# Kernel tuning notes

Hardware: AMD Instinct MI355X
Metric: run time of the kernel (lower is better)

Reference implementation:

```python
import jax, jax.numpy as jnp
import numpy as np

IN_DIM = 1024
OUT_DIM = 1024
NUM_EXPERTS = 8
TOP_K = 2
B = 8192


def setup_inputs() -> dict:
    key = jax.random.key(0)
    ks = jax.random.split(key, 8)
    s_in = 1.0 / np.sqrt(IN_DIM)
    s_out = 1.0 / np.sqrt(OUT_DIM)
    return {
        "x": jax.random.normal(ks[0], (B, IN_DIM), dtype=jnp.float32),
        # router Linear(in_dim, num_experts)
        "rw": jax.random.uniform(ks[1], (IN_DIM, NUM_EXPERTS), jnp.float32, -s_in, s_in),
        "rb": jax.random.uniform(ks[2], (NUM_EXPERTS,), jnp.float32, -s_in, s_in),
        # expert MLPs stacked along expert axis
        "w1": jax.random.uniform(ks[3], (NUM_EXPERTS, IN_DIM, OUT_DIM), jnp.float32, -s_in, s_in),
        "b1": jax.random.uniform(ks[4], (NUM_EXPERTS, OUT_DIM), jnp.float32, -s_in, s_in),
        "w2": jax.random.uniform(ks[5], (NUM_EXPERTS, OUT_DIM, OUT_DIM), jnp.float32, -s_out, s_out),
        "b2": jax.random.uniform(ks[6], (NUM_EXPERTS, OUT_DIM), jnp.float32, -s_out, s_out),
    }


def reference(x, rw, rb, w1, b1, w2, b2):
    # ---- TopkRouter ----
    logits = x @ rw + rb                                  # [B, E]
    topk_vals, topk_idx = jax.lax.top_k(logits, TOP_K)    # [B, K]
    neg_inf = jnp.full_like(logits, -jnp.inf)
    rows = jnp.arange(logits.shape[0])[:, None]
    sparse_logits = neg_inf.at[rows, topk_idx].set(topk_vals)
    gating = jax.nn.softmax(sparse_logits, axis=-1)       # zeros outside top-k

    # ---- experts: dense compute, gating weights are exactly 0 for
    # non-selected experts so the weighted combine matches the masked
    # dispatch of the original module. ----
    h = jax.nn.relu(jnp.einsum('bi,eio->beo', x, w1) + b1[None])   # [B, E, out]
    y = jnp.einsum('beh,eho->beo', h, w2) + b2[None]               # [B, E, out]
    fused = jnp.einsum('beo,be->bo', y, gating)                    # [B, out]
    return fused, gating
```

## Files before the change

### kernel.cpp

```cpp
#include <hip/hip_runtime.h>
#include <hip/hip_bf16.h>
#include <cstdint>
#include <cstddef>

#define IN_DIM 1024
#define OUT_DIM 1024
#define NE 8
#define NTOK 8192

typedef __bf16 bf16x8 __attribute__((ext_vector_type(8)));
typedef float f32x4 __attribute__((ext_vector_type(4)));

__device__ __forceinline__ unsigned short f2bf(float f) {
    unsigned u = __float_as_uint(f);
    unsigned r = 0x7fffu + ((u >> 16) & 1u);
    return (unsigned short)((u + r) >> 16);
}

__device__ __forceinline__ void bf2x(unsigned u, float& lo, float& hi) {
    lo = __uint_as_float(u << 16);
    hi = __uint_as_float(u & 0xffff0000u);
}

__device__ __forceinline__ void async16(void* lds, const void* g) {
    __builtin_amdgcn_global_load_lds(
        (const __attribute__((address_space(1))) unsigned int*)g,
        (__attribute__((address_space(3))) unsigned int*)lds,
        16, 0, 0);
}

__global__ __launch_bounds__(256) void convert_transpose_kernel(
    const float* __restrict__ w1, const float* __restrict__ w2,
    unsigned short* __restrict__ w1T, unsigned short* __restrict__ w2T) {
    __shared__ float tile[64][68];
    int z = blockIdx.z;
    const float* src = (z < 8) ? (w1 + (size_t)z * IN_DIM * OUT_DIM)
                               : (w2 + (size_t)(z - 8) * OUT_DIM * OUT_DIM);
    unsigned short* dst = (z < 8) ? (w1T + (size_t)z * IN_DIM * OUT_DIM)
                                  : (w2T + (size_t)(z - 8) * OUT_DIM * OUT_DIM);
    int kt = blockIdx.x * 64, nt = blockIdx.y * 64;
    int t = threadIdx.x;
    int r = t >> 2, cq = (t & 3) * 16;
#pragma unroll
    for (int q = 0; q < 4; ++q) {
        float4 v = *(const float4*)(src + (size_t)(kt + r) * 1024 + nt + cq + q * 4);
        tile[r][cq + q * 4 + 0] = v.x;
        tile[r][cq + q * 4 + 1] = v.y;
        tile[r][cq + q * 4 + 2] = v.z;
        tile[r][cq + q * 4 + 3] = v.w;
    }
    __syncthreads();
    int n = t >> 2, kq = (t & 3) * 16;
#pragma unroll
    for (int q = 0; q < 4; ++q) {
        ushort4 o;
        o.x = f2bf(tile[kq + q * 4 + 0][n]);
        o.y = f2bf(tile[kq + q * 4 + 1][n]);
        o.z = f2bf(tile[kq + q * 4 + 2][n]);
        o.w = f2bf(tile[kq + q * 4 + 3][n]);
        *(ushort4*)(dst + (size_t)(nt + n) * 1024 + kt + kq + q * 4) = o;
    }
}

__global__ __launch_bounds__(256) void router_kernel(
    const float* __restrict__ x, const float* __restrict__ rw,
    const float* __restrict__ rb,
    unsigned short* __restrict__ xb,
    float* __restrict__ gating, int* __restrict__ enc,
    float2* __restrict__ gw) {
    __shared__ float srw[NE * IN_DIM];
    int t = threadIdx.x;
#pragma unroll
    for (int i = 0; i < 4; ++i) {
        int k = t + i * 256;
        float4 a = *(const float4*)(rw + (size_t)k * NE);
        float4 b = *(const float4*)(rw + (size_t)k * NE + 4);
        srw[0 * IN_DIM + k] = a.x; srw[1 * IN_DIM + k] = a.y;
        srw[2 * IN_DIM + k] = a.z; srw[3 * IN_DIM + k] = a.w;
        srw[4 * IN_DIM + k] = b.x; srw[5 * IN_DIM + k] = b.y;
        srw[6 * IN_DIM + k] = b.z; srw[7 * IN_DIM + k] = b.w;
    }
    __syncthreads();
    int wave = t >> 6, lane = t & 63;
    int tok = blockIdx.x * 4 + wave;
    const float* xrow = x + (size_t)tok * IN_DIM;
    unsigned short* xbrow = xb + (size_t)tok * IN_DIM;
    float acc[NE] = {0, 0, 0, 0, 0, 0, 0, 0};
#pragma unroll
    for (int i = 0; i < 4; ++i) {
        int k = i * 256 + lane * 4;
        float4 xv = *(const float4*)(xrow + k);
        ushort4 o;
        o.x = f2bf(xv.x); o.y = f2bf(xv.y); o.z = f2bf(xv.z); o.w = f2bf(xv.w);
        *(ushort4*)(xbrow + k) = o;
#pragma unroll
        for (int e = 0; e < NE; ++e) {
            float4 wv = *(const float4*)(srw + e * IN_DIM + k);
            acc[e] = fmaf(xv.x, wv.x, fmaf(xv.y, wv.y, fmaf(xv.z, wv.z, fmaf(xv.w, wv.w, acc[e]))));
        }
    }
#pragma unroll
    for (int e = 0; e < NE; ++e) {
#pragma unroll
        for (int off = 32; off > 0; off >>= 1) acc[e] += __shfl_xor(acc[e], off);
        acc[e] += rb[e];
    }
    int e0 = 0; float v0 = acc[0];
#pragma unroll
    for (int e = 1; e < NE; ++e) if (acc[e] > v0) { v0 = acc[e]; e0 = e; }
    int e1 = -1; float v1 = -3.4e38f;
#pragma unroll
    for (int e = 0; e < NE; ++e) if (e != e0 && acc[e] > v1) { v1 = acc[e]; e1 = e; }
    float tg = __expf(v1 - v0);
    float inv = 1.0f / (1.0f + tg);
    float g0 = inv, g1 = tg * inv;
    if (lane < NE) gating[(size_t)tok * NE + lane] = (lane == e0) ? g0 : ((lane == e1) ? g1 : 0.0f);
    if (lane == 0) {
        enc[tok] = e0 | (e1 << 8);
        gw[tok] = make_float2(g0, g1);
    }
}

__global__ __launch_bounds__(1024) void bucket_kernel(
    const int* __restrict__ enc,
    int* __restrict__ bidx, int* __restrict__ slots, int* __restrict__ cnt) {
    int e = blockIdx.x;
    __shared__ int wsum[16];
    __shared__ int runbase;
    int t = threadIdx.x, wave = t >> 6, lane = t & 63;
    if (t == 0) runbase = 0;
    __syncthreads();
    for (int c0 = 0; c0 < NTOK; c0 += 1024) {
        int tok = c0 + t;
        int v = enc[tok];
        int e0 = v & 0xff, e1 = (v >> 8) & 0xff;
        bool sel = (e0 == e) || (e1 == e);
        unsigned long long m = __ballot(sel);
        int pos = __popcll(m & ((1ull << lane) - 1ull));
        if (lane == 0) wsum[wave] = __popcll(m);
        __syncthreads();
        int wb = runbase;
        for (int w = 0; w < wave; ++w) wb += wsum[w];
        if (sel) {
            int p = wb + pos;
            bidx[e * NTOK + p] = tok;
            int which = (e0 == e) ? 0 : 1;
            slots[2 * tok + which] = (e << 13) | p;
        }
        __syncthreads();
        if (t == 0) {
            int s = 0;
#pragma unroll
            for (int w = 0; w < 16; ++w) s += wsum[w];
            runbase += s;
        }
        __syncthreads();
    }
    if (t == 0) cnt[e] = runbase;
}

__device__ __forceinline__ int prefix_cnt(const int* __restrict__ cnt, int e) {
    int s = 0;
    for (int i = 0; i < NE; ++i) s += (i < e) ? cnt[i] : 0;
    return s;
}


__global__ __launch_bounds__(256) void gemm1_kernel(
    const unsigned short* __restrict__ xb, const unsigned short* __restrict__ w1T,
    const float* __restrict__ b1, const int* __restrict__ bidx,
    const int* __restrict__ cnt,
    unsigned short* __restrict__ H) {
    int b = blockIdx.x;
    int e = b & 7;
    int t2 = b >> 3;
    int nt = t2 & 7;
    int mt = t2 >> 3;
    int n_e = cnt[e];
    if (mt * 128 >= n_e) return;
    __shared__ __attribute__((aligned(16))) unsigned short As[2][64 * 64];
    __shared__ __attribute__((aligned(16))) unsigned short Bs[2][64 * 64];
    int t = threadIdx.x, wave = t >> 6, lane = t & 63;
    const int* be = bidx + e * NTOK;
    const unsigned short* agp[2]; const unsigned short* bgp[2];
    int ldsoff[2];
#pragma unroll
    for (int is = 0; is < 2; ++is) {
        int c = is * 256 + t;
        int line = c >> 3;
        int chunkg = (c & 7) ^ (line & 7);
        int growl = 2 * line + (chunkg >> 2);
        int gcol = (chunkg & 3) * 8;
        int gra = mt * 128 + growl;
        int grac = gra < n_e ? gra : n_e - 1;
        agp[is] = xb + (size_t)be[grac] * IN_DIM + gcol;
        bgp[is] = w1T + ((size_t)e * OUT_DIM + nt * 128 + growl) * IN_DIM + gcol;
        ldsoff[is] = (is * 256 + wave * 64) * 8;
    }
    int wm = wave & 1, wn = wave >> 1;
    int quad = lane >> 4, l15 = lane & 15;
    int lhalf = l15 >> 1;
    int slot = (((l15 & 1) * 4 + quad) ^ lhalf) * 8;
    f32x4 zero4 = {0.f, 0.f, 0.f, 0.f};
    f32x4 acc[4][4];
#pragma unroll
    for (int i = 0; i < 4; ++i)
#pragma unroll
        for (int j = 0; j < 4; ++j) acc[i][j] = zero4;

#pragma unroll
    for (int is = 0; is < 2; ++is) {
        async16(&As[0][ldsoff[is]], agp[is]);
        async16(&Bs[0][ldsoff[is]], bgp[is]);
    }
    for (int it = 0; it < 32; ++it) {
        __syncthreads();
        int buf = it & 1;
        if (it + 1 < 32) {
            int ktn = (it + 1) * 32;
#pragma unroll
            for (int is = 0; is < 2; ++is) {
                async16(&As[buf ^ 1][ldsoff[is]], agp[is] + ktn);
                async16(&Bs[buf ^ 1][ldsoff[is]], bgp[is] + ktn);
            }
        }
        const unsigned short* Ab = As[buf];
        const unsigned short* Bb = Bs[buf];
        bf16x8 av[4], bv[4];
#pragma unroll
        for (int i = 0; i < 4; ++i) {
            int lineA = wm * 32 + i * 8 + lhalf;
            av[i] = *(const bf16x8*)(Ab + lineA * 64 + slot);
        }
#pragma unroll
        for (int j = 0; j < 4; ++j) {
            int lineB = wn * 32 + j * 8 + lhalf;
            bv[j] = *(const bf16x8*)(Bb + lineB * 64 + slot);
        }
#pragma unroll
        for (int i = 0; i < 4; ++i)
#pragma unroll
            for (int j = 0; j < 4; ++j)
                acc[i][j] = __builtin_amdgcn_mfma_f32_16x16x32_bf16(av[i], bv[j], acc[i][j], 0, 0, 0);
    }
    int hbase = prefix_cnt(cnt, e);
    const float* b1e = b1 + (size_t)e * OUT_DIM;
    int n0 = nt * 128 + wn * 64 + l15;
#pragma unroll
    for (int j = 0; j < 4; ++j) {
        int n = n0 + j * 16;
        float bias = b1e[n];
#pragma unroll
        for (int i = 0; i < 4; ++i) {
            int m0 = mt * 128 + wm * 64 + i * 16 + quad * 4;
#pragma unroll
            for (int r = 0; r < 4; ++r) {
                int gm = m0 + r;
                if (gm < n_e) {
                    float h = acc[i][j][r] + bias;
                    h = h > 0.f ? h : 0.f;
                    H[(size_t)(hbase + gm) * OUT_DIM + n] = f2bf(h);
                }
            }
        }
    }
}

__global__ __launch_bounds__(256) void gemm2_kernel(
    const unsigned short* __restrict__ H, const unsigned short* __restrict__ w2T,
    const int* __restrict__ cnt,
    unsigned short* __restrict__ Y) {
    int b = blockIdx.x;
    int e = b & 7;
    int t2 = b >> 3;
    int nt = t2 & 7;
    int mt = t2 >> 3;
    int n_e = cnt[e];
    if (mt * 128 >= n_e) return;
    __shared__ __attribute__((aligned(16))) unsigned short As[2][64 * 64];
    __shared__ __attribute__((aligned(16))) unsigned short Bs[2][64 * 64];
    int t = threadIdx.x, wave = t >> 6, lane = t & 63;
    int hbase = prefix_cnt(cnt, e);
    const unsigned short* agp[2]; const unsigned short* bgp[2];
    int ldsoff[2];
#pragma unroll
    for (int is = 0; is < 2; ++is) {
        int c = is * 256 + t;
        int line = c >> 3;
        int chunkg = (c & 7) ^ (line & 7);
        int growl = 2 * line + (chunkg >> 2);
        int gcol = (chunkg & 3) * 8;
        int gra = mt * 128 + growl;
        int grac = gra < n_e ? gra : n_e - 1;
        agp[is] = H + (size_t)(hbase + grac) * OUT_DIM + gcol;
        bgp[is] = w2T + ((size_t)e * OUT_DIM + nt * 128 + growl) * OUT_DIM + gcol;
        ldsoff[is] = (is * 256 + wave * 64) * 8;
    }
    int wm = wave & 1, wn = wave >> 1;
    int quad = lane >> 4, l15 = lane & 15;
    int lhalf = l15 >> 1;
    int slot = (((l15 & 1) * 4 + quad) ^ lhalf) * 8;
    f32x4 zero4 = {0.f, 0.f, 0.f, 0.f};
    f32x4 acc[4][4];
#pragma unroll
    for (int i = 0; i < 4; ++i)
#pragma unroll
        for (int j = 0; j < 4; ++j) acc[i][j] = zero4;

#pragma unroll
    for (int is = 0; is < 2; ++is) {
        async16(&As[0][ldsoff[is]], agp[is]);
        async16(&Bs[0][ldsoff[is]], bgp[is]);
    }
    for (int it = 0; it < 32; ++it) {
        __syncthreads();
        int buf = it & 1;
        if (it + 1 < 32) {
            int ktn = (it + 1) * 32;
#pragma unroll
            for (int is = 0; is < 2; ++is) {
                async16(&As[buf ^ 1][ldsoff[is]], agp[is] + ktn);
                async16(&Bs[buf ^ 1][ldsoff[is]], bgp[is] + ktn);
            }
        }
        const unsigned short* Ab = As[buf];
        const unsigned short* Bb = Bs[buf];
        bf16x8 av[4], bv[4];
#pragma unroll
        for (int i = 0; i < 4; ++i) {
            int lineA = wm * 32 + i * 8 + lhalf;
            av[i] = *(const bf16x8*)(Ab + lineA * 64 + slot);
        }
#pragma unroll
        for (int j = 0; j < 4; ++j) {
            int lineB = wn * 32 + j * 8 + lhalf;
            bv[j] = *(const bf16x8*)(Bb + lineB * 64 + slot);
        }
#pragma unroll
        for (int i = 0; i < 4; ++i)
#pragma unroll
            for (int j = 0; j < 4; ++j)
                acc[i][j] = __builtin_amdgcn_mfma_f32_16x16x32_bf16(av[i], bv[j], acc[i][j], 0, 0, 0);
    }
    int n0 = nt * 128 + wn * 64 + l15;
#pragma unroll
    for (int i = 0; i < 4; ++i) {
        int m0 = mt * 128 + wm * 64 + i * 16 + quad * 4;
#pragma unroll
        for (int r = 0; r < 4; ++r) {
            int gm = m0 + r;
            if (gm < n_e) {
                unsigned short* yrow = Y + (size_t)(hbase + gm) * OUT_DIM;
#pragma unroll
                for (int j = 0; j < 4; ++j)
                    yrow[n0 + j * 16] = f2bf(acc[i][j][r]);
            }
        }
    }
}

__global__ __launch_bounds__(256) void combine_kernel(
    const unsigned short* __restrict__ Y, const float* __restrict__ b2,
    const float2* __restrict__ gw, const int* __restrict__ slots,
    const int* __restrict__ cnt, float* __restrict__ out) {
    int t = threadIdx.x, wave = t >> 6, lane = t & 63;
    int tok = blockIdx.x * 4 + wave;
    int pre[NE];
    {
        int s = 0;
#pragma unroll
        for (int i = 0; i < NE; ++i) { pre[i] = s; s += cnt[i]; }
    }
    int s0 = slots[2 * tok], s1 = slots[2 * tok + 1];
    int e0 = s0 >> 13, e1 = s1 >> 13;
    int r0 = pre[e0] + (s0 & 8191);
    int r1 = pre[e1] + (s1 & 8191);
    float2 g = gw[tok];
    const unsigned short* y0 = Y + (size_t)r0 * OUT_DIM;
    const unsigned short* y1 = Y + (size_t)r1 * OUT_DIM;
    const float* c0 = b2 + (size_t)e0 * OUT_DIM;
    const float* c1 = b2 + (size_t)e1 * OUT_DIM;
    float* orow = out + (size_t)tok * OUT_DIM;
#pragma unroll
    for (int i = 0; i < 2; ++i) {
        int c = i * 512 + lane * 8;
        uint4 ua = *(const uint4*)(y0 + c);
        uint4 ub = *(const uint4*)(y1 + c);
        float a[8], b[8];
        bf2x(ua.x, a[0], a[1]); bf2x(ua.y, a[2], a[3]);
        bf2x(ua.z, a[4], a[5]); bf2x(ua.w, a[6], a[7]);
        bf2x(ub.x, b[0], b[1]); bf2x(ub.y, b[2], b[3]);
        bf2x(ub.z, b[4], b[5]); bf2x(ub.w, b[6], b[7]);
        float4 p0 = *(const float4*)(c0 + c);
        float4 p1 = *(const float4*)(c0 + c + 4);
        float4 q0 = *(const float4*)(c1 + c);
        float4 q1 = *(const float4*)(c1 + c + 4);
        float o[8];
        o[0] = g.x * (a[0] + p0.x) + g.y * (b[0] + q0.x);
        o[1] = g.x * (a[1] + p0.y) + g.y * (b[1] + q0.y);
        o[2] = g.x * (a[2] + p0.z) + g.y * (b[2] + q0.z);
        o[3] = g.x * (a[3] + p0.w) + g.y * (b[3] + q0.w);
        o[4] = g.x * (a[4] + p1.x) + g.y * (b[4] + q1.x);
        o[5] = g.x * (a[5] + p1.y) + g.y * (b[5] + q1.y);
        o[6] = g.x * (a[6] + p1.z) + g.y * (b[6] + q1.z);
        o[7] = g.x * (a[7] + p1.w) + g.y * (b[7] + q1.w);
        *(float4*)(orow + c) = make_float4(o[0], o[1], o[2], o[3]);
        *(float4*)(orow + c + 4) = make_float4(o[4], o[5], o[6], o[7]);
    }
}

extern "C" void kernel_launch(void* const* d_in, const int* in_sizes, int n_in,
                              void* d_out, int out_size, void* d_ws, size_t ws_size,
                              hipStream_t stream) {
    const float* x  = (const float*)d_in[0];
    const float* rw = (const float*)d_in[1];
    const float* rb = (const float*)d_in[2];
    const float* w1 = (const float*)d_in[3];
    const float* b1 = (const float*)d_in[4];
    const float* w2 = (const float*)d_in[5];
    const float* b2 = (const float*)d_in[6];
    float* out = (float*)d_out;
    float* gating = out + (size_t)NTOK * OUT_DIM;

    char* ws = (char*)d_ws;
    unsigned short* xb  = (unsigned short*)(ws + 0);
    unsigned short* Y   = (unsigned short*)(ws + 0);
    unsigned short* w1T = (unsigned short*)(ws + 16777216);
    unsigned short* w2T = (unsigned short*)(ws + 33554432);
    unsigned short* H   = (unsigned short*)(ws + 50331648);
    int*   bidx  = (int*)(ws + 83886080);
    int*   slots = (int*)(ws + 84148224);
    int*   cnt   = (int*)(ws + 84213760);
    int*    enc  = (int*)(ws + 84213888);
    float2* gw   = (float2*)(ws + 84246656);

    convert_transpose_kernel<<<dim3(16, 16, 16), 256, 0, stream>>>(w1, w2, w1T, w2T);
    router_kernel<<<NTOK / 4, 256, 0, stream>>>(x, rw, rb, xb, gating, enc, gw);
    bucket_kernel<<<NE, 1024, 0, stream>>>(enc, bidx, slots, cnt);
    gemm1_kernel<<<8 * 8 * 64, 256, 0, stream>>>(xb, w1T, b1, bidx, cnt, H);
    gemm2_kernel<<<8 * 8 * 64, 256, 0, stream>>>(H, w2T, cnt, Y);
    combine_kernel<<<NTOK / 4, 256, 0, stream>>>(Y, b2, gw, slots, cnt, out);
    (void)in_sizes; (void)n_in; (void)out_size; (void)ws_size;
}
```

Before: 310.6 us.

## Parallelize expert bucketing with atomics and vectorize GEMM epilogue stores

The bucket kernel changes from one block per expert scanning all tokens to one thread per token, using wave ballots plus an atomicAdd on the per-expert counters, which the router now zeroes. The GEMM B-tile rows are permuted so each lane owns four adjacent output columns, letting the bias load and the H and Y stores become 4-wide vector accesses instead of scattered 2-byte writes. The weight convert-transpose now writes 8-wide vectors. Token order within each expert bucket now depends on atomic ordering and is no longer deterministic, though each token's slot stays consistent.

```diff
diff --git a/kernel.cpp b/kernel.cpp
--- a/kernel.cpp
+++ b/kernel.cpp
@@ -10,6 +10,7 @@
 
 typedef __bf16 bf16x8 __attribute__((ext_vector_type(8)));
 typedef float f32x4 __attribute__((ext_vector_type(4)));
+typedef unsigned short ushort8v __attribute__((ext_vector_type(8)));
 
 __device__ __forceinline__ unsigned short f2bf(float f) {
     unsigned u = __float_as_uint(f);
@@ -52,13 +53,11 @@
     __syncthreads();
     int n = t >> 2, kq = (t & 3) * 16;
 #pragma unroll
-    for (int q = 0; q < 4; ++q) {
-        ushort4 o;
-        o.x = f2bf(tile[kq + q * 4 + 0][n]);
-        o.y = f2bf(tile[kq + q * 4 + 1][n]);
-        o.z = f2bf(tile[kq + q * 4 + 2][n]);
-        o.w = f2bf(tile[kq + q * 4 + 3][n]);
-        *(ushort4*)(dst + (size_t)(nt + n) * 1024 + kt + kq + q * 4) = o;
+    for (int q = 0; q < 2; ++q) {
+        ushort8v o;
+#pragma unroll
+        for (int i = 0; i < 8; ++i) o[i] = f2bf(tile[kq + q * 8 + i][n]);
+        *(ushort8v*)(dst + (size_t)(nt + n) * 1024 + kt + kq + q * 8) = o;
     }
 }
 
@@ -67,9 +66,10 @@
     const float* __restrict__ rb,
     unsigned short* __restrict__ xb,
     float* __restrict__ gating, int* __restrict__ enc,
-    float2* __restrict__ gw) {
+    float2* __restrict__ gw, int* __restrict__ cnt) {
     __shared__ float srw[NE * IN_DIM];
     int t = threadIdx.x;
+    if (blockIdx.x == 0 && t < NE) cnt[t] = 0;
 #pragma unroll
     for (int i = 0; i < 4; ++i) {
         int k = t + i * 256;
@@ -121,42 +121,30 @@
     }
 }
 
-__global__ __launch_bounds__(1024) void bucket_kernel(
+__global__ __launch_bounds__(256) void bucket_kernel(
     const int* __restrict__ enc,
     int* __restrict__ bidx, int* __restrict__ slots, int* __restrict__ cnt) {
-    int e = blockIdx.x;
-    __shared__ int wsum[16];
-    __shared__ int runbase;
-    int t = threadIdx.x, wave = t >> 6, lane = t & 63;
-    if (t == 0) runbase = 0;
-    __syncthreads();
-    for (int c0 = 0; c0 < NTOK; c0 += 1024) {
-        int tok = c0 + t;
-        int v = enc[tok];
-        int e0 = v & 0xff, e1 = (v >> 8) & 0xff;
-        bool sel = (e0 == e) || (e1 == e);
-        unsigned long long m = __ballot(sel);
-        int pos = __popcll(m & ((1ull << lane) - 1ull));
-        if (lane == 0) wsum[wave] = __popcll(m);
-        __syncthreads();
-        int wb = runbase;
-        for (int w = 0; w < wave; ++w) wb += wsum[w];
-        if (sel) {
-            int p = wb + pos;
-            bidx[e * NTOK + p] = tok;
-            int which = (e0 == e) ? 0 : 1;
-            slots[2 * tok + which] = (e << 13) | p;
-        }
-        __syncthreads();
-        if (t == 0) {
-            int s = 0;
-#pragma unroll
-            for (int w = 0; w < 16; ++w) s += wsum[w];
-            runbase += s;
-        }
-        __syncthreads();
-    }
-    if (t == 0) cnt[e] = runbase;
+    int tok = blockIdx.x * 256 + threadIdx.x;
+    int lane = threadIdx.x & 63;
+    int v = enc[tok];
+    int e0 = v & 0xff, e1 = (v >> 8) & 0xff;
+    unsigned long long below = (1ull << lane) - 1ull;
+    int p0 = 0, p1 = 0;
+#pragma unroll
+    for (int e = 0; e < NE; ++e) {
+        unsigned long long m0 = __ballot(e0 == e);
+        unsigned long long m1 = __ballot(e1 == e);
+        int c0 = __popcll(m0), c1 = __popcll(m1);
+        int base = 0;
+        if (lane == 0 && (c0 + c1)) base = atomicAdd(&cnt[e], c0 + c1);
+        base = __shfl(base, 0);
+        if (e0 == e) p0 = base + __popcll(m0 & below);
+        if (e1 == e) p1 = base + c0 + __popcll(m1 & below);
+    }
+    bidx[e0 * NTOK + p0] = tok;
+    bidx[e1 * NTOK + p1] = tok;
+    slots[2 * tok + 0] = (e0 << 13) | p0;
+    slots[2 * tok + 1] = (e1 << 13) | p1;
 }
 
 __device__ __forceinline__ int prefix_cnt(const int* __restrict__ cnt, int e) {
@@ -189,12 +177,14 @@
         int c = is * 256 + t;
         int line = c >> 3;
         int chunkg = (c & 7) ^ (line & 7);
-        int growl = 2 * line + (chunkg >> 2);
+        int sub = chunkg >> 2;
+        int growl = 2 * line + sub;
+        int growlB = (line >> 5) * 64 + (line & 7) * 8 + sub * 4 + ((line >> 3) & 3);
         int gcol = (chunkg & 3) * 8;
         int gra = mt * 128 + growl;
         int grac = gra < n_e ? gra : n_e - 1;
         agp[is] = xb + (size_t)be[grac] * IN_DIM + gcol;
-        bgp[is] = w1T + ((size_t)e * OUT_DIM + nt * 128 + growl) * IN_DIM + gcol;
+        bgp[is] = w1T + ((size_t)e * OUT_DIM + nt * 128 + growlB) * IN_DIM + gcol;
         ldsoff[is] = (is * 256 + wave * 64) * 8;
     }
     int wm = wave & 1, wn = wave >> 1;
@@ -245,22 +235,22 @@
     }
     int hbase = prefix_cnt(cnt, e);
     const float* b1e = b1 + (size_t)e * OUT_DIM;
-    int n0 = nt * 128 + wn * 64 + l15;
-#pragma unroll
-    for (int j = 0; j < 4; ++j) {
-        int n = n0 + j * 16;
-        float bias = b1e[n];
-#pragma unroll
-        for (int i = 0; i < 4; ++i) {
-            int m0 = mt * 128 + wm * 64 + i * 16 + quad * 4;
-#pragma unroll
-            for (int r = 0; r < 4; ++r) {
-                int gm = m0 + r;
-                if (gm < n_e) {
-                    float h = acc[i][j][r] + bias;
-                    h = h > 0.f ? h : 0.f;
-                    H[(size_t)(hbase + gm) * OUT_DIM + n] = f2bf(h);
-                }
+    int n0 = nt * 128 + wn * 64 + l15 * 4;
+    float4 bias = *(const float4*)(b1e + n0);
+#pragma unroll
+    for (int i = 0; i < 4; ++i) {
+        int m0 = mt * 128 + wm * 64 + i * 16 + quad * 4;
+#pragma unroll
+        for (int r = 0; r < 4; ++r) {
+            int gm = m0 + r;
+            if (gm < n_e) {
+                float h0 = acc[i][0][r] + bias.x; h0 = h0 > 0.f ? h0 : 0.f;
+                float h1 = acc[i][1][r] + bias.y; h1 = h1 > 0.f ? h1 : 0.f;
+                float h2 = acc[i][2][r] + bias.z; h2 = h2 > 0.f ? h2 : 0.f;
+                float h3 = acc[i][3][r] + bias.w; h3 = h3 > 0.f ? h3 : 0.f;
+                ushort4 o;
+                o.x = f2bf(h0); o.y = f2bf(h1); o.z = f2bf(h2); o.w = f2bf(h3);
+                *(ushort4*)(H + (size_t)(hbase + gm) * OUT_DIM + n0) = o;
             }
         }
     }
@@ -288,12 +278,14 @@
         int c = is * 256 + t;
         int line = c >> 3;
         int chunkg = (c & 7) ^ (line & 7);
-        int growl = 2 * line + (chunkg >> 2);
+        int sub = chunkg >> 2;
+        int growl = 2 * line + sub;
+        int growlB = (line >> 5) * 64 + (line & 7) * 8 + sub * 4 + ((line >> 3) & 3);
         int gcol = (chunkg & 3) * 8;
         int gra = mt * 128 + growl;
         int grac = gra < n_e ? gra : n_e - 1;
         agp[is] = H + (size_t)(hbase + grac) * OUT_DIM + gcol;
-        bgp[is] = w2T + ((size_t)e * OUT_DIM + nt * 128 + growl) * OUT_DIM + gcol;
+        bgp[is] = w2T + ((size_t)e * OUT_DIM + nt * 128 + growlB) * OUT_DIM + gcol;
         ldsoff[is] = (is * 256 + wave * 64) * 8;
     }
     int wm = wave & 1, wn = wave >> 1;
@@ -342,7 +334,7 @@
             for (int j = 0; j < 4; ++j)
                 acc[i][j] = __builtin_amdgcn_mfma_f32_16x16x32_bf16(av[i], bv[j], acc[i][j], 0, 0, 0);
     }
-    int n0 = nt * 128 + wn * 64 + l15;
+    int n0 = nt * 128 + wn * 64 + l15 * 4;
 #pragma unroll
     for (int i = 0; i < 4; ++i) {
         int m0 = mt * 128 + wm * 64 + i * 16 + quad * 4;
@@ -350,10 +342,10 @@
         for (int r = 0; r < 4; ++r) {
             int gm = m0 + r;
             if (gm < n_e) {
-                unsigned short* yrow = Y + (size_t)(hbase + gm) * OUT_DIM;
-#pragma unroll
-                for (int j = 0; j < 4; ++j)
-                    yrow[n0 + j * 16] = f2bf(acc[i][j][r]);
+                ushort4 o;
+                o.x = f2bf(acc[i][0][r]); o.y = f2bf(acc[i][1][r]);
+                o.z = f2bf(acc[i][2][r]); o.w = f2bf(acc[i][3][r]);
+                *(ushort4*)(Y + (size_t)(hbase + gm) * OUT_DIM + n0) = o;
             }
         }
     }
@@ -435,8 +427,8 @@
     float2* gw   = (float2*)(ws + 84246656);
 
     convert_transpose_kernel<<<dim3(16, 16, 16), 256, 0, stream>>>(w1, w2, w1T, w2T);
-    router_kernel<<<NTOK / 4, 256, 0, stream>>>(x, rw, rb, xb, gating, enc, gw);
-    bucket_kernel<<<NE, 1024, 0, stream>>>(enc, bidx, slots, cnt);
+    router_kernel<<<NTOK / 4, 256, 0, stream>>>(x, rw, rb, xb, gating, enc, gw, cnt);
+    bucket_kernel<<<NTOK / 256, 256, 0, stream>>>(enc, bidx, slots, cnt);
     gemm1_kernel<<<8 * 8 * 64, 256, 0, stream>>>(xb, w1T, b1, bidx, cnt, H);
     gemm2_kernel<<<8 * 8 * 64, 256, 0, stream>>>(H, w2T, cnt, Y);
     combine_kernel<<<NTOK / 4, 256, 0, stream>>>(Y, b2, gw, slots, cnt, out);
```

Result: faster. 298.4 us (-3.9%).
